# Optimization experiments

Measured on AMD Instinct MI355X. Metric: run time of the kernel, lower is better.

## Reference

```python
import jax, jax.numpy as jnp
import numpy as np

RADIUS = 1.0
B, D, L = 4096, 256, 3

def setup_inputs() -> dict:
    key = jax.random.key(0)
    k1, k2 = jax.random.split(key)
    feature_space = jax.random.normal(k1, (B, D), dtype=jnp.float32)
    labels = jax.random.randint(k2, (B, L), 0, 8, dtype=jnp.int64)
    return {"feature_space": feature_space, "labels": labels}

def reference(feature_space, labels):
    sq = jnp.sum(feature_space * feature_space, axis=-1)            # [B]
    gram = feature_space @ feature_space.T                           # [B, B]
    d2 = jnp.maximum(sq[:, None] + sq[None, :] - 2.0 * gram, 0.0)   # [B, B]
    # safe sqrt (diagonal / duplicate points have d2 == 0)
    dist = jnp.where(d2 > 0, jnp.sqrt(jnp.where(d2 > 0, d2, 1.0)), 0.0)
    same = jnp.all(labels[:, None, :] == labels[None, :, :], axis=-1).astype(feature_space.dtype)  # [B, B]
    # per-pair contrastive term
    term = 0.5 * same * dist + 0.5 * (1.0 - same) * jnp.maximum(RADIUS - dist, 0.0)
    # only i < j pairs (strict upper triangle)
    n = feature_space.shape[0]
    mask = jnp.triu(jnp.ones((n, n), dtype=feature_space.dtype), k=1)
    loss = jnp.sum(term * mask) / n
    return loss.reshape(1)  # torch returns a shape-[1] tensor
```

## Files before the change

### kernel.cpp

```cpp
#include <hip/hip_runtime.h>

#define B_N 4096
#define D_K 256
#define BT  64
#define NT  (B_N / BT)
#define NBLK (NT * (NT + 1) / 2)
#define BK  64
#define NKITER (D_K / BK)

typedef __bf16 bf16x8 __attribute__((ext_vector_type(8)));
typedef float  floatx4 __attribute__((ext_vector_type(4)));

typedef __attribute__((address_space(3))) unsigned int lds_u32;
typedef const __attribute__((address_space(1))) unsigned int glb_u32;

__device__ inline unsigned short f2bf(float f) {
    unsigned int u = __float_as_uint(f);
    return (unsigned short)((u + 0x7FFFu + ((u >> 16) & 1u)) >> 16);
}

__global__ __launch_bounds__(256) void prep_kernel(const float* __restrict__ F,
                                                   const int* __restrict__ labels,
                                                   float* __restrict__ sq,
                                                   int* __restrict__ plab,
                                                   unsigned short* __restrict__ Fb) {
    int row  = blockIdx.x * 4 + (threadIdx.x >> 6);
    int lane = threadIdx.x & 63;
    const float4* fp = reinterpret_cast<const float4*>(F + (size_t)row * D_K);
    float4 v = fp[lane];
    ushort4 b;
    b.x = f2bf(v.x); b.y = f2bf(v.y); b.z = f2bf(v.z); b.w = f2bf(v.w);
    reinterpret_cast<ushort4*>(Fb + (size_t)row * D_K)[lane] = b;
    float s = v.x * v.x + v.y * v.y + v.z * v.z + v.w * v.w;
#pragma unroll
    for (int off = 32; off > 0; off >>= 1) s += __shfl_down(s, off);
    if (lane == 0) {
        sq[row] = s;
        const int* lp = labels + (size_t)row * 3;
        plab[row] = lp[0] | (lp[1] << 3) | (lp[2] << 6);
    }
}

__global__ __launch_bounds__(256) void pair_kernel(const unsigned short* __restrict__ Fb,
                                                   const float* __restrict__ sq,
                                                   const int* __restrict__ plab,
                                                   float* __restrict__ partials) {
    __shared__ unsigned short smem[2 * BT * BK];
    __shared__ float red[4];

    int idx = blockIdx.x, bi = 0;
    while (idx >= NT - bi) { idx -= NT - bi; ++bi; }
    const int bj = bi + idx;
    const bool diag = (bi == bj);

    const int i0   = bi * BT;
    const int j0   = bj * BT;
    const int wave = threadIdx.x >> 6;
    const int lane = threadIdx.x & 63;
    const int lrow = lane & 15;
    const int kgrp = lane >> 4;
    const int r0   = (wave >> 1) * 32;
    const int c0   = (wave & 1) * 32;

    char* lAs = (char*)smem;
    char* lBs = diag ? lAs : (char*)(smem + BT * BK);

    floatx4 acc[2][2];
#pragma unroll
    for (int tm = 0; tm < 2; ++tm)
#pragma unroll
        for (int tn = 0; tn < 2; ++tn) acc[tm][tn] = floatx4{0.f, 0.f, 0.f, 0.f};

    const int srow_in = lane >> 3;
    const int sphys   = lane & 7;

    const char* gA = (const char*)(Fb + (size_t)i0 * D_K);
    const char* gB = (const char*)(Fb + (size_t)j0 * D_K);

    for (int it = 0; it < NKITER; ++it) {
        const size_t kbyte = (size_t)it * BK * 2;
#pragma unroll
        for (int q = 0; q < 2; ++q) {
            int instr = wave * 2 + q;
            int row   = instr * 8 + srow_in;
            int chunk = sphys ^ (row & 7);
            __builtin_amdgcn_global_load_lds(
                (glb_u32*)(gA + (size_t)row * (D_K * 2) + kbyte + chunk * 16),
                (lds_u32*)(lAs + instr * 1024), 16, 0, 0);
            if (!diag)
                __builtin_amdgcn_global_load_lds(
                    (glb_u32*)(gB + (size_t)row * (D_K * 2) + kbyte + chunk * 16),
                    (lds_u32*)(lBs + instr * 1024), 16, 0, 0);
        }
        __syncthreads();

#pragma unroll
        for (int ks = 0; ks < 2; ++ks) {
            bf16x8 a[2], b[2];
            const int c = ks * 4 + kgrp;
#pragma unroll
            for (int tm = 0; tm < 2; ++tm) {
                int row = r0 + tm * 16 + lrow;
                a[tm] = *reinterpret_cast<const bf16x8*>(
                    lAs + row * 128 + ((c ^ (row & 7)) * 16));
            }
#pragma unroll
            for (int tn = 0; tn < 2; ++tn) {
                int row = c0 + tn * 16 + lrow;
                b[tn] = *reinterpret_cast<const bf16x8*>(
                    lBs + row * 128 + ((c ^ (row & 7)) * 16));
            }
#pragma unroll
            for (int tm = 0; tm < 2; ++tm)
#pragma unroll
                for (int tn = 0; tn < 2; ++tn)
                    acc[tm][tn] = __builtin_amdgcn_mfma_f32_16x16x32_bf16(
                        a[tm], b[tn], acc[tm][tn], 0, 0, 0);
        }
        __syncthreads();
    }

    float sqj[2];
    int   lj[2];
#pragma unroll
    for (int tn = 0; tn < 2; ++tn) {
        int j = j0 + c0 + tn * 16 + lrow;
        sqj[tn] = sq[j];
        lj[tn]  = plab[j];
    }

    float local = 0.f;
#pragma unroll
    for (int tm = 0; tm < 2; ++tm) {
#pragma unroll
        for (int r = 0; r < 4; ++r) {
            int i = i0 + r0 + tm * 16 + kgrp * 4 + r;
            float sqi = sq[i];
            int   li  = plab[i];
#pragma unroll
            for (int tn = 0; tn < 2; ++tn) {
                int j = j0 + c0 + tn * 16 + lrow;
                if (j > i) {
                    float d2 = fmaxf(sqi + sqj[tn] - 2.f * acc[tm][tn][r], 0.f);
                    float dist = sqrtf(d2);
                    local += (li == lj[tn]) ? (0.5f * dist)
                                            : (0.5f * fmaxf(1.f - dist, 0.f));
                }
            }
        }
    }

#pragma unroll
    for (int off = 32; off > 0; off >>= 1) local += __shfl_down(local, off);
    if (lane == 0) red[wave] = local;
    __syncthreads();
    if (threadIdx.x == 0)
        partials[blockIdx.x] = red[0] + red[1] + red[2] + red[3];
}

__global__ __launch_bounds__(256) void reduce_kernel(const float* __restrict__ partials,
                                                     float* __restrict__ out) {
    __shared__ float red[4];
    float s = 0.f;
    for (int i = threadIdx.x; i < NBLK; i += 256) s += partials[i];
#pragma unroll
    for (int off = 32; off > 0; off >>= 1) s += __shfl_down(s, off);
    if ((threadIdx.x & 63) == 0) red[threadIdx.x >> 6] = s;
    __syncthreads();
    if (threadIdx.x == 0)
        out[0] = (red[0] + red[1] + red[2] + red[3]) * (1.0f / B_N);
}

extern "C" void kernel_launch(void* const* d_in, const int* in_sizes, int n_in,
                              void* d_out, int out_size, void* d_ws, size_t ws_size,
                              hipStream_t stream) {
    const float* F      = (const float*)d_in[0];
    const int*   labels = (const int*)d_in[1];
    float* out = (float*)d_out;

    float*          sq    = (float*)d_ws;
    int*            plab  = (int*)((char*)d_ws + B_N * 4);
    float*          parts = (float*)((char*)d_ws + 2 * B_N * 4);
    unsigned short* Fb    = (unsigned short*)((char*)d_ws + 65536);

    prep_kernel<<<B_N / 4, 256, 0, stream>>>(F, labels, sq, plab, Fb);
    pair_kernel<<<NBLK, 256, 0, stream>>>(Fb, sq, plab, parts);
    reduce_kernel<<<1, 256, 0, stream>>>(parts, out);
}
```

Baseline: 75.54 us.

## Double-buffer LDS tiles and fold final reduction into pair kernel via last-block atomic

Splits the shared-memory tiles into two buffers so the global-to-LDS load of the next K slice is issued before the MFMAs on the current slice, leaving one barrier per iteration instead of two. It also removes the separate reduce launch: each block writes its partial atomically, bumps a counter that prep_kernel resets, and the last block sums all partials and writes the output. This saves one kernel launch and some barrier stalls, at the cost of twice the LDS per block (which may lower occupancy) and extra atomic traffic.

```diff
diff --git a/kernel.cpp b/kernel.cpp
--- a/kernel.cpp
+++ b/kernel.cpp
@@ -23,7 +23,9 @@
                                                    const int* __restrict__ labels,
                                                    float* __restrict__ sq,
                                                    int* __restrict__ plab,
-                                                   unsigned short* __restrict__ Fb) {
+                                                   unsigned short* __restrict__ Fb,
+                                                   unsigned int* __restrict__ counter) {
+    if (blockIdx.x == 0 && threadIdx.x == 0) *counter = 0;
     int row  = blockIdx.x * 4 + (threadIdx.x >> 6);
     int lane = threadIdx.x & 63;
     const float4* fp = reinterpret_cast<const float4*>(F + (size_t)row * D_K);
@@ -44,9 +46,13 @@
 __global__ __launch_bounds__(256) void pair_kernel(const unsigned short* __restrict__ Fb,
                                                    const float* __restrict__ sq,
                                                    const int* __restrict__ plab,
-                                                   float* __restrict__ partials) {
-    __shared__ unsigned short smem[2 * BT * BK];
+                                                   float* __restrict__ partials,
+                                                   unsigned int* __restrict__ counter,
+                                                   float* __restrict__ out) {
+    __shared__ unsigned short As[2][BT * BK];
+    __shared__ unsigned short Bs[2][BT * BK];
     __shared__ float red[4];
+    __shared__ bool  amLast;
 
     int idx = blockIdx.x, bi = 0;
     while (idx >= NT - bi) { idx -= NT - bi; ++bi; }
@@ -62,9 +68,6 @@
     const int r0   = (wave >> 1) * 32;
     const int c0   = (wave & 1) * 32;
 
-    char* lAs = (char*)smem;
-    char* lBs = diag ? lAs : (char*)(smem + BT * BK);
-
     floatx4 acc[2][2];
 #pragma unroll
     for (int tm = 0; tm < 2; ++tm)
@@ -77,8 +80,10 @@
     const char* gA = (const char*)(Fb + (size_t)i0 * D_K);
     const char* gB = (const char*)(Fb + (size_t)j0 * D_K);
 
-    for (int it = 0; it < NKITER; ++it) {
+    auto stage = [&](int it, int buf) {
         const size_t kbyte = (size_t)it * BK * 2;
+        char* lAs = (char*)As[buf];
+        char* lBs = (char*)Bs[buf];
 #pragma unroll
         for (int q = 0; q < 2; ++q) {
             int instr = wave * 2 + q;
@@ -92,8 +97,17 @@
                     (glb_u32*)(gB + (size_t)row * (D_K * 2) + kbyte + chunk * 16),
                     (lds_u32*)(lBs + instr * 1024), 16, 0, 0);
         }
+    };
+
+    stage(0, 0);
+
+    for (int it = 0; it < NKITER; ++it) {
+        const int cur = it & 1;
         __syncthreads();
-
+        if (it + 1 < NKITER) stage(it + 1, cur ^ 1);
+
+        const char* cAs = (const char*)As[cur];
+        const char* cBs = diag ? cAs : (const char*)Bs[cur];
 #pragma unroll
         for (int ks = 0; ks < 2; ++ks) {
             bf16x8 a[2], b[2];
@@ -102,13 +116,13 @@
             for (int tm = 0; tm < 2; ++tm) {
                 int row = r0 + tm * 16 + lrow;
                 a[tm] = *reinterpret_cast<const bf16x8*>(
-                    lAs + row * 128 + ((c ^ (row & 7)) * 16));
+                    cAs + row * 128 + ((c ^ (row & 7)) * 16));
             }
 #pragma unroll
             for (int tn = 0; tn < 2; ++tn) {
                 int row = c0 + tn * 16 + lrow;
                 b[tn] = *reinterpret_cast<const bf16x8*>(
-                    lBs + row * 128 + ((c ^ (row & 7)) * 16));
+                    cBs + row * 128 + ((c ^ (row & 7)) * 16));
             }
 #pragma unroll
             for (int tm = 0; tm < 2; ++tm)
@@ -117,7 +131,6 @@
                     acc[tm][tn] = __builtin_amdgcn_mfma_f32_16x16x32_bf16(
                         a[tm], b[tn], acc[tm][tn], 0, 0, 0);
         }
-        __syncthreads();
     }
 
     float sqj[2];
@@ -154,21 +167,27 @@
     for (int off = 32; off > 0; off >>= 1) local += __shfl_down(local, off);
     if (lane == 0) red[wave] = local;
     __syncthreads();
-    if (threadIdx.x == 0)
-        partials[blockIdx.x] = red[0] + red[1] + red[2] + red[3];
-}
-
-__global__ __launch_bounds__(256) void reduce_kernel(const float* __restrict__ partials,
-                                                     float* __restrict__ out) {
-    __shared__ float red[4];
-    float s = 0.f;
-    for (int i = threadIdx.x; i < NBLK; i += 256) s += partials[i];
-#pragma unroll
-    for (int off = 32; off > 0; off >>= 1) s += __shfl_down(s, off);
-    if ((threadIdx.x & 63) == 0) red[threadIdx.x >> 6] = s;
+
+    if (threadIdx.x == 0) {
+        float bsum = red[0] + red[1] + red[2] + red[3];
+        float old = atomicExch(&partials[blockIdx.x], bsum);
+        __asm__ volatile("" : "+v"(old));
+        unsigned int done = atomicAdd(counter, 1u);
+        amLast = (done == NBLK - 1);
+    }
     __syncthreads();
-    if (threadIdx.x == 0)
-        out[0] = (red[0] + red[1] + red[2] + red[3]) * (1.0f / B_N);
+
+    if (amLast) {
+        float s = 0.f;
+        for (int i = threadIdx.x; i < NBLK; i += 256)
+            s += atomicAdd(&partials[i], 0.0f);
+#pragma unroll
+        for (int off = 32; off > 0; off >>= 1) s += __shfl_down(s, off);
+        if (lane == 0) red[wave] = s;
+        __syncthreads();
+        if (threadIdx.x == 0)
+            out[0] = (red[0] + red[1] + red[2] + red[3]) * (1.0f / B_N);
+    }
 }
 
 extern "C" void kernel_launch(void* const* d_in, const int* in_sizes, int n_in,
@@ -181,9 +200,9 @@
     float*          sq    = (float*)d_ws;
     int*            plab  = (int*)((char*)d_ws + B_N * 4);
     float*          parts = (float*)((char*)d_ws + 2 * B_N * 4);
+    unsigned int*   cnt   = (unsigned int*)((char*)d_ws + 48 * 1024);
     unsigned short* Fb    = (unsigned short*)((char*)d_ws + 65536);
 
-    prep_kernel<<<B_N / 4, 256, 0, stream>>>(F, labels, sq, plab, Fb);
-    pair_kernel<<<NBLK, 256, 0, stream>>>(Fb, sq, plab, parts);
-    reduce_kernel<<<1, 256, 0, stream>>>(parts, out);
-}
+    prep_kernel<<<B_N / 4, 256, 0, stream>>>(F, labels, sq, plab, Fb, cnt);
+    pair_kernel<<<NBLK, 256, 0, stream>>>(Fb, sq, plab, parts, cnt, out);
+}
```

Result: slower. 93.02 us (+23.1%).
